# Kernel optimization log

Measured on AMD Instinct MI355X. Metric: run time of the kernel, lower is better.

The kernel has to match this reference:

```python
import jax, jax.numpy as jnp
import numpy as np

NUM_HEADS = 8
HEAD_DIM = 64      # key_dim = tts_embed_dims // num_heads
TOKEN_NUM = 10
EMBED_DIMS = 512   # tts_embed_dims (num_units)
QUERY_DIM = 256    # tts_embed_dims // 2
BATCH = 131072


def setup_inputs() -> dict:
    key = jax.random.key(0)
    k1, k2, k3, k4 = jax.random.split(key, 4)
    inputs = jax.random.normal(k1, (BATCH, QUERY_DIM), dtype=jnp.float32)
    # nn.Parameter init.normal_(mean=0, std=0.5)
    embed = 0.5 * jax.random.normal(k2, (TOKEN_NUM, HEAD_DIM), dtype=jnp.float32)
    # nn.Linear weights are [out_features, in_features]
    Wq = jax.random.normal(k3, (EMBED_DIMS, QUERY_DIM), dtype=jnp.float32) * (QUERY_DIM ** -0.5)
    Wk = jax.random.normal(k4, (EMBED_DIMS, HEAD_DIM), dtype=jnp.float32) * (HEAD_DIM ** -0.5)
    return {"inputs": inputs, "embed": embed, "Wq": Wq, "Wk": Wk}


def reference(inputs, embed, Wq, Wk):
    # Faithful to this fork: values = raw tanh(embed) keys (W_value unused),
    # and NO softmax on the attention scores.
    N = inputs.shape[0]
    h, d, T = NUM_HEADS, HEAD_DIM, TOKEN_NUM
    keys_raw = jnp.tanh(embed)                       # [T, d] (shared across batch)

    q = inputs @ Wq.T                                # [N, E]
    q = q.reshape(N, h, d)                           # split heads (T_q == 1 squeezed)

    k = keys_raw @ Wk.T                              # [T, E]
    k = k.reshape(T, h, d)                           # [T, h, d]

    scale = HEAD_DIM ** 0.5                          # self.key_dim ** 0.5
    # scores: [h, N, 1, T] -> store as [h, N, T]
    scores = jnp.einsum('nhd,thd->hnt', q, k) / scale

    # out per head: scores @ values, values = keys_raw [T, d]
    out = jnp.einsum('hnt,td->nhd', scores, keys_raw)  # [N, h, d]
    style_embed = out.reshape(N, 1, h * d)             # concat heads -> [N, 1, E]
    attn_score = scores[:, :, None, :]                 # [h, N, 1, T]
    return style_embed, attn_score
```

## Files before the change

### kernel.cpp

```cpp
#include <hip/hip_runtime.h>
#include <math.h>

#define N_QDIM 256
#define N_EDIM 512
#define N_HEADS 8
#define N_HDIM 64
#define N_TOK 10
#define NJ 80

typedef short bf16x8 __attribute__((ext_vector_type(8)));
typedef float f32x4 __attribute__((ext_vector_type(4)));

__global__ __launch_bounds__(256) void precompute_kernel(
    const float* __restrict__ embed, const float* __restrict__ Wq,
    const float* __restrict__ Wk, unsigned short* __restrict__ WfHi,
    unsigned short* __restrict__ WfLo, float* __restrict__ keysOut)
{
    __shared__ float skeys[N_TOK * N_HDIM];
    __shared__ float sK[N_TOK * N_EDIM];
    const int tid = threadIdx.x;

    for (int i = tid; i < N_TOK * N_HDIM; i += 256) {
        float v = tanhf(embed[i]);
        skeys[i] = v;
        if (blockIdx.x == 0) keysOut[i] = v;
    }
    __syncthreads();

    for (int i = tid; i < N_TOK * N_EDIM; i += 256) {
        int t = i >> 9;
        int e = i & 511;
        float s = 0.f;
        #pragma unroll
        for (int d = 0; d < N_HDIM; d++)
            s += skeys[t * N_HDIM + d] * Wk[e * N_HDIM + d];
        sK[i] = s;
    }
    __syncthreads();

    int flat = blockIdx.x * 256 + tid;
    int e    = flat & 7;
    int lane = (flat >> 3) & 63;
    int rest = flat >> 9;
    int n    = rest % 5;
    int kb   = rest / 5;
    int c    = n * 16 + (lane & 15);
    int h    = c / N_TOK;
    int t    = c - h * N_TOK;
    int qd   = kb * 32 + (lane >> 4) * 8 + e;

    float s = 0.f;
    #pragma unroll
    for (int d = 0; d < N_HDIM; d++)
        s += Wq[(h * N_HDIM + d) * N_QDIM + qd] * sK[t * N_EDIM + h * N_HDIM + d];
    s *= 0.125f;

    unsigned int u = __float_as_uint(s);
    float rem = s - __uint_as_float(u & 0xffff0000u);
    int idx = ((kb * 5 + n) * 64 + lane) * 8 + e;
    WfHi[idx] = (unsigned short)(u >> 16);
    WfLo[idx] = (unsigned short)(__float_as_uint(rem) >> 16);
}

static __device__ __forceinline__ void splitFrag(float4 v0, float4 v1,
                                                 bf16x8& hi, bf16x8& lo)
{
    float x[8] = {v0.x, v0.y, v0.z, v0.w, v1.x, v1.y, v1.z, v1.w};
    #pragma unroll
    for (int e = 0; e < 8; e++) {
        unsigned u = __float_as_uint(x[e]);
        hi[e] = (short)(u >> 16);
        float r = x[e] - __uint_as_float(u & 0xffff0000u);
        lo[e] = (short)(__float_as_uint(r) >> 16);
    }
}

__global__ __launch_bounds__(256, 4) void main_kernel(
    const float* __restrict__ inputs, const unsigned short* __restrict__ WfHi,
    const unsigned short* __restrict__ WfLo, const float* __restrict__ keys,
    float* __restrict__ outStyle, float* __restrict__ outAttn, int N)
{
    __shared__ float sS[4][16 * 84];

    const int tid = threadIdx.x;
    const int w   = tid >> 6;
    const int l   = tid & 63;
    const int l15 = l & 15;
    const int lg  = l >> 4;
    const int rowBase = blockIdx.x * 128 + w * 32;

    const float* pa0 = inputs + (size_t)(rowBase + l15) * N_QDIM + lg * 8;
    const float* pa1 = pa0 + 16 * N_QDIM;

    f32x4 acc[2][5];
    #pragma unroll
    for (int m = 0; m < 2; m++)
        #pragma unroll
        for (int n = 0; n < 5; n++)
            acc[m][n] = (f32x4){0.f, 0.f, 0.f, 0.f};

    #pragma unroll 2
    for (int kb = 0; kb < 8; kb++) {
        const float* p0 = pa0 + kb * 32;
        const float* p1 = pa1 + kb * 32;
        float4 x0 = *(const float4*)(p0);
        float4 x1 = *(const float4*)(p0 + 4);
        float4 y0 = *(const float4*)(p1);
        float4 y1 = *(const float4*)(p1 + 4);
        bf16x8 a0h, a0l, a1h, a1l;
        splitFrag(x0, x1, a0h, a0l);
        splitFrag(y0, y1, a1h, a1l);

        const unsigned short* bh = WfHi + kb * 2560 + l * 8;
        const unsigned short* bl = WfLo + kb * 2560 + l * 8;
        #pragma unroll
        for (int n = 0; n < 5; n++) {
            bf16x8 bhi = *(const bf16x8*)(bh + n * 512);
            bf16x8 blo = *(const bf16x8*)(bl + n * 512);
            acc[0][n] = __builtin_amdgcn_mfma_f32_16x16x32_bf16(a0h, bhi, acc[0][n], 0, 0, 0);
            acc[1][n] = __builtin_amdgcn_mfma_f32_16x16x32_bf16(a1h, bhi, acc[1][n], 0, 0, 0);
            acc[0][n] = __builtin_amdgcn_mfma_f32_16x16x32_bf16(a0l, bhi, acc[0][n], 0, 0, 0);
            acc[1][n] = __builtin_amdgcn_mfma_f32_16x16x32_bf16(a1l, bhi, acc[1][n], 0, 0, 0);
            acc[0][n] = __builtin_amdgcn_mfma_f32_16x16x32_bf16(a0h, blo, acc[0][n], 0, 0, 0);
            acc[1][n] = __builtin_amdgcn_mfma_f32_16x16x32_bf16(a1h, blo, acc[1][n], 0, 0, 0);
        }
    }

    float4 kr[N_TOK];
    #pragma unroll
    for (int t = 0; t < N_TOK; t++)
        kr[t] = *(const float4*)(keys + t * N_HDIM + l15 * 4);

    float* s = sS[w];

    #pragma unroll
    for (int m = 0; m < 2; m++) {
        #pragma unroll
        for (int n = 0; n < 5; n++)
            #pragma unroll
            for (int r = 0; r < 4; r++)
                s[(lg * 4 + r) * 84 + n * 16 + l15] = acc[m][n][r];
        __syncthreads();

        const int rStart = rowBase + m * 16;

        #pragma unroll
        for (int h = 0; h < N_HEADS; h++) {
            float* dst = outAttn + ((size_t)h * N + rStart) * N_TOK;
            for (int i = l; i < 16 * N_TOK; i += 64) {
                int rr = i / N_TOK;
                int t  = i - rr * N_TOK;
                dst[i] = s[rr * 84 + h * N_TOK + t];
            }
        }

        #pragma unroll
        for (int i = 0; i < 4; i++) {
            int rr = i * 4 + lg;
            const float* srow = s + rr * 84;
            float* orow = outStyle + (size_t)(rStart + rr) * N_EDIM + l15 * 4;
            #pragma unroll
            for (int h = 0; h < N_HEADS; h++) {
                float4 o = {0.f, 0.f, 0.f, 0.f};
                #pragma unroll
                for (int t2 = 0; t2 < N_TOK; t2 += 2) {
                    float2 sc = *(const float2*)(srow + h * N_TOK + t2);
                    o.x += sc.x * kr[t2].x + sc.y * kr[t2 + 1].x;
                    o.y += sc.x * kr[t2].y + sc.y * kr[t2 + 1].y;
                    o.z += sc.x * kr[t2].z + sc.y * kr[t2 + 1].z;
                    o.w += sc.x * kr[t2].w + sc.y * kr[t2 + 1].w;
                }
                *(float4*)(orow + h * N_HDIM) = o;
            }
        }
        __syncthreads();
    }
}

extern "C" void kernel_launch(void* const* d_in, const int* in_sizes, int n_in,
                              void* d_out, int out_size, void* d_ws, size_t ws_size,
                              hipStream_t stream) {
    const float* inputs = (const float*)d_in[0];
    const float* embed  = (const float*)d_in[1];
    const float* Wq     = (const float*)d_in[2];
    const float* Wk     = (const float*)d_in[3];

    const int N = in_sizes[0] / N_QDIM;

    float* keysWs = (float*)d_ws;
    unsigned short* WfHi = (unsigned short*)((char*)d_ws + 640 * sizeof(float));
    unsigned short* WfLo = WfHi + 8 * 5 * 64 * 8;

    float* outStyle = (float*)d_out;
    float* outAttn  = outStyle + (size_t)N * N_EDIM;

    precompute_kernel<<<80, 256, 0, stream>>>(embed, Wq, Wk, WfHi, WfLo, keysWs);
    main_kernel<<<N / 128, 256, 0, stream>>>(inputs, WfHi, WfLo, keysWs, outStyle, outAttn, N);
}
```

Baseline: 457.1 us.

## Replace block barriers with wave-local LDS fences, add nontemporal stores, raise occupancy

Each wave uses its own shared-memory slice, so the block-wide __syncthreads calls in the epilogue are replaced with s_waitcnt lgkmcnt(0) fences that only order a wave's own LDS traffic. The output stores for both style embeddings and attention scores now use nontemporal stores to avoid polluting caches with write-once data. The launch bounds minimum blocks per CU is raised from 4 to 5, and the attention store loop is fully unrolled. The risks are register spills under the tighter bound and reliance on wave-level lockstep for LDS visibility.

```diff
diff --git a/kernel.cpp b/kernel.cpp
--- a/kernel.cpp
+++ b/kernel.cpp
@@ -75,7 +75,9 @@
     }
 }
 
-__global__ __launch_bounds__(256, 4) void main_kernel(
+#define WAVE_LDS_FENCE() asm volatile("s_waitcnt lgkmcnt(0)" ::: "memory")
+
+__global__ __launch_bounds__(256, 5) void main_kernel(
     const float* __restrict__ inputs, const unsigned short* __restrict__ WfHi,
     const unsigned short* __restrict__ WfLo, const float* __restrict__ keys,
     float* __restrict__ outStyle, float* __restrict__ outAttn, int N)
@@ -126,31 +128,35 @@
         }
     }
 
+    float* s = sS[w];
+
+    #pragma unroll
+    for (int n = 0; n < 5; n++)
+        #pragma unroll
+        for (int r = 0; r < 4; r++)
+            s[(lg * 4 + r) * 84 + n * 16 + l15] = acc[0][n][r];
+    WAVE_LDS_FENCE();
+
     float4 kr[N_TOK];
     #pragma unroll
     for (int t = 0; t < N_TOK; t++)
         kr[t] = *(const float4*)(keys + t * N_HDIM + l15 * 4);
 
-    float* s = sS[w];
-
     #pragma unroll
     for (int m = 0; m < 2; m++) {
-        #pragma unroll
-        for (int n = 0; n < 5; n++)
-            #pragma unroll
-            for (int r = 0; r < 4; r++)
-                s[(lg * 4 + r) * 84 + n * 16 + l15] = acc[m][n][r];
-        __syncthreads();
-
         const int rStart = rowBase + m * 16;
 
         #pragma unroll
         for (int h = 0; h < N_HEADS; h++) {
             float* dst = outAttn + ((size_t)h * N + rStart) * N_TOK;
-            for (int i = l; i < 16 * N_TOK; i += 64) {
-                int rr = i / N_TOK;
-                int t  = i - rr * N_TOK;
-                dst[i] = s[rr * 84 + h * N_TOK + t];
+            #pragma unroll
+            for (int it = 0; it < 3; it++) {
+                int i = it * 64 + l;
+                if (i < 16 * N_TOK) {
+                    int rr = i / N_TOK;
+                    int t  = i - rr * N_TOK;
+                    __builtin_nontemporal_store(s[rr * 84 + h * N_TOK + t], dst + i);
+                }
             }
         }
 
@@ -161,19 +167,28 @@
             float* orow = outStyle + (size_t)(rStart + rr) * N_EDIM + l15 * 4;
             #pragma unroll
             for (int h = 0; h < N_HEADS; h++) {
-                float4 o = {0.f, 0.f, 0.f, 0.f};
+                f32x4 o = {0.f, 0.f, 0.f, 0.f};
                 #pragma unroll
                 for (int t2 = 0; t2 < N_TOK; t2 += 2) {
                     float2 sc = *(const float2*)(srow + h * N_TOK + t2);
-                    o.x += sc.x * kr[t2].x + sc.y * kr[t2 + 1].x;
-                    o.y += sc.x * kr[t2].y + sc.y * kr[t2 + 1].y;
-                    o.z += sc.x * kr[t2].z + sc.y * kr[t2 + 1].z;
-                    o.w += sc.x * kr[t2].w + sc.y * kr[t2 + 1].w;
+                    o[0] += sc.x * kr[t2].x + sc.y * kr[t2 + 1].x;
+                    o[1] += sc.x * kr[t2].y + sc.y * kr[t2 + 1].y;
+                    o[2] += sc.x * kr[t2].z + sc.y * kr[t2 + 1].z;
+                    o[3] += sc.x * kr[t2].w + sc.y * kr[t2 + 1].w;
                 }
-                *(float4*)(orow + h * N_HDIM) = o;
+                __builtin_nontemporal_store(o, (f32x4*)(orow + h * N_HDIM));
             }
         }
-        __syncthreads();
+
+        if (m == 0) {
+            WAVE_LDS_FENCE();
+            #pragma unroll
+            for (int n = 0; n < 5; n++)
+                #pragma unroll
+                for (int r = 0; r < 4; r++)
+                    s[(lg * 4 + r) * 84 + n * 16 + l15] = acc[1][n][r];
+            WAVE_LDS_FENCE();
+        }
     }
 }
 
```

Result: no change. 463.8 us (+1.5%).
